# Kernel optimization log

Hardware: AMD Instinct MI355X
Metric: run time of the kernel (lower is better)

Reference implementation:

```python
import jax, jax.numpy as jnp
import numpy as np

V, C, L, D = 16384, 16, 6, 64  # n_vars, max_clauses, max_variables, embedding_dim


def _normalize(x):
    # utils.normalize: L2-normalize along the feature axis
    return x / jnp.linalg.norm(x, axis=-1, keepdims=True)


def _rescombine(x, W1, b1, W2, b2):
    # ResidualCombine: normalize(sigmoid(layer1(x)) + layer2(x))
    h = jax.nn.sigmoid(x @ W1 + b1) + x @ W2 + b2
    return _normalize(h)


def setup_inputs() -> dict:
    key = jax.random.key(0)
    ks = jax.random.split(key, 14)
    s = 0.05
    variables = jax.random.normal(ks[0], (V, D), jnp.float32)
    # literal variable indices; slot 0 of every clause is the owning variable i
    lits = jax.random.randint(ks[1], (V, C, L), 0, V)
    lits = lits.at[:, :, 0].set(jnp.arange(V)[:, None])
    neg_mask = jax.random.bernoulli(ks[2], 0.5, (V, C, L))
    # literal validity: at least 2 literals per clause, slot 0 always valid
    nvar = jax.random.randint(ks[3], (V, C), 2, L + 1)
    var_valid = jnp.arange(L)[None, None, :] < nvar[:, :, None]
    # clause validity: at least 1 clause per variable
    nclause = jax.random.randint(ks[4], (V,), 1, C + 1)
    clause_valid = jnp.arange(C)[None, :] < nclause[:, None]
    # params
    Wn = jax.random.normal(ks[5], (D, D), jnp.float32) * s
    bn = jnp.zeros((D,), jnp.float32)
    f = jax.random.normal(ks[6], (D,), jnp.float32)
    false_emb = f / jnp.linalg.norm(f)  # Embedding(1, D, max_norm=1.0)
    W1v = jax.random.normal(ks[7], (L * D, D), jnp.float32) * s
    b1v = jnp.zeros((D,), jnp.float32)
    W2v = jax.random.normal(ks[8], (L * D, D), jnp.float32) * s
    b2v = jnp.zeros((D,), jnp.float32)
    W1c = jax.random.normal(ks[9], (C * D, D), jnp.float32) * s
    b1c = jnp.zeros((D,), jnp.float32)
    W2c = jax.random.normal(ks[10], (C * D, D), jnp.float32) * s
    b2c = jnp.zeros((D,), jnp.float32)
    return dict(variables=variables, lits=lits, neg_mask=neg_mask, var_valid=var_valid,
                clause_valid=clause_valid, Wn=Wn, bn=bn, false_emb=false_emb,
                W1v=W1v, b1v=b1v, W2v=W2v, b2v=b2v, W1c=W1c, b1c=b1c, W2c=W2c, b2c=b2c)


def reference(variables, lits, neg_mask, var_valid, clause_valid,
              Wn, bn, false_emb, W1v, b1v, W2v, b2v, W1c, b1c, W2c, b2c):
    # gather literal embeddings: [V, C, L, D]
    g = variables[lits]
    # negation linear for negative literals
    v = jnp.where(neg_mask[..., None], g @ Wn + bn, g)
    # pad invalid literal slots with the 'false' embedding
    v = jnp.where(var_valid[..., None], v, false_emb)
    # variable_combiner over flattened [L*D]
    clause_emb = _rescombine(v.reshape(V, C, L * D), W1v, b1v, W2v, b2v)  # [V, C, D]
    # pad missing clauses with 'true' = negation(false)
    true_emb = false_emb @ Wn + bn
    clause_emb = jnp.where(clause_valid[..., None], clause_emb, true_emb)
    # clause_combiner over flattened [C*D]
    out = _rescombine(clause_emb.reshape(V, C * D), W1c, b1c, W2c, b2c)  # [V, D]
    # variables with no clauses pass through unchanged
    has_clauses = clause_valid.any(axis=-1)
    return jnp.where(has_clauses[:, None], out, variables)
```

## Files before the change

### kernel.cpp

```cpp
#include <hip/hip_runtime.h>
#include <hip/hip_bf16.h>

#define NV 16384
#define NC 16
#define NL 6
#define ND 64

typedef unsigned short u16;
typedef unsigned int u32;
typedef __attribute__((ext_vector_type(8))) short short8;
typedef __attribute__((ext_vector_type(4))) float f32x4;

#define PB_BN  0
#define PB_FE  64
#define PB_B1V 128
#define PB_B2V 192
#define PB_B1C 256
#define PB_B2C 320
#define U_BVS   896
#define U_BCS   50048
#define U_BN    181120
#define U_VARSB 185216
#define U_NEGB  1233856
#define U_CES   2282496
#define U_FIDX  19059712

__device__ __forceinline__ float ldbf(const u16* p, int i) {
  return __uint_as_float(((u32)p[i]) << 16);
}
__device__ __forceinline__ u16 f2b(float f) {
  u32 x = __float_as_uint(f);
  return (u16)((x + 0x7FFF + ((x >> 16) & 1)) >> 16);
}
__device__ __forceinline__ int ldmask(const void* p, int i, int bdt) {
  return bdt ? (int)((const signed char*)p)[i] : ((const int*)p)[i];
}
__device__ __forceinline__ float ldf(const void* p, int i, int fdt) {
  return fdt ? ldbf((const u16*)p, i) : ((const float*)p)[i];
}
__device__ __forceinline__ void gll16(const u16* g, u16* l) {
  __builtin_amdgcn_global_load_lds(
      (const __attribute__((address_space(1))) u32*)(g),
      (__attribute__((address_space(3))) u32*)(l), 16, 0, 0);
}

__global__ __launch_bounds__(256) void k_prep(
    const void* vars, const int* __restrict__ lits, const void* negm, const void* vval,
    const void* Wn, const void* bn, const void* femb,
    const void* W1v, const void* b1v, const void* W2v, const void* b2v,
    const void* W1c, const void* b1c, const void* W2c, const void* b2c,
    int* flags, float* pbuf, u16* wsB) {
  __shared__ int s_cnt[4], s_big[4];
  const int t = threadIdx.x;
  {
    const u32 w = ((const u32*)vars)[t];
    const u32 e = (w >> 7) & 0xFF;
    const unsigned long long bal = __ballot(e >= 0x6E && e <= 0x8E);
    const u32 bw = ((const u32*)vval)[t];
    const unsigned long long bb = __ballot(bw > 1u);
    if ((t & 63) == 0) { s_cnt[t >> 6] = __popcll(bal); s_big[t >> 6] = (bb != 0ull); }
  }
  __syncthreads();
  const int fdt = (s_cnt[0] + s_cnt[1] + s_cnt[2] + s_cnt[3]) >= 192;
  const int bdt = (s_big[0] | s_big[1] | s_big[2] | s_big[3]);
  const int bid = blockIdx.x;

  if (bid == 0) {
    if (t == 0) { flags[0] = fdt; flags[1] = bdt; }
    if (t < 64) {
      const void* src[6] = {bn, femb, b1v, b2v, b1c, b2c};
      const int off[6] = {PB_BN, PB_FE, PB_B1V, PB_B2V, PB_B1C, PB_B2C};
      for (int j = 0; j < 6; j++) pbuf[off[j] + t] = ldf(src[j], t, fdt);
      wsB[U_VARSB + NV * 64 + t] = fdt ? ((const u16*)femb)[t] : f2b(((const float*)femb)[t]);
    }
    for (int i = t; i < 4096; i += 256) {
      const int n = i >> 6, k = i & 63;
      wsB[U_BN + i] = f2b(ldf(Wn, k * 64 + n, fdt));
    }
  } else if (bid < 25) {
    const int c = (bid - 1) * 256 + t;
    const int ln = c & 63, nt = (c >> 6) & 7, ks = c >> 9;
    const int n = nt * 16 + (ln & 15);
    const void* src = (n < 64) ? W1v : W2v;
    const int kb = ks * 32 + (ln >> 4) * 8, n6 = n & 63;
    u16 o[8];
#pragma unroll
    for (int j = 0; j < 8; j++) o[j] = f2b(ldf(src, (kb + j) * 64 + n6, fdt));
    *(short8*)(wsB + U_BVS + c * 8) = *(short8*)o;
  } else if (bid < 89) {
    const int c = (bid - 25) * 256 + t;
    const int ln = c & 63, nt = (c >> 6) & 7, ks = c >> 9;
    const int n = nt * 16 + (ln & 15);
    const void* src = (n < 64) ? W1c : W2c;
    const int kb = ks * 32 + (ln >> 4) * 8, n6 = n & 63;
    u16 o[8];
#pragma unroll
    for (int j = 0; j < 8; j++) o[j] = f2b(ldf(src, (kb + j) * 64 + n6, fdt));
    *(short8*)(wsB + U_BCS + c * 8) = *(short8*)o;
  } else if (bid < 601) {
    const int c8 = (bid - 89) * 256 + t;
    u16 o[8];
    if (fdt) {
      *(short8*)o = ((const short8*)vars)[c8];
    } else {
      const float* f = (const float*)vars + c8 * 8;
#pragma unroll
      for (int j = 0; j < 8; j++) o[j] = f2b(f[j]);
    }
    *(short8*)(wsB + U_VARSB + c8 * 8) = *(short8*)o;
  } else {
    const int i0 = ((bid - 601) * 256 + t) * 4;
    u16 o[4];
#pragma unroll
    for (int j = 0; j < 4; j++) {
      const int i = i0 + j;
      const int valid = ldmask(vval, i, bdt);
      const int neg = ldmask(negm, i, bdt);
      const int idx = lits[i];
      o[j] = (u16)(valid ? (idx + (neg ? (NV + 1) : 0)) : NV);
    }
    *(ushort4*)(wsB + U_FIDX + i0) = *(ushort4*)o;
  }
}

__global__ __launch_bounds__(256) void k_negvar(const float* pbuf, u16* wsB) {
  const int tid = threadIdx.x, lane = tid & 63, wv = tid >> 6;
  const int col = lane & 15, quad = lane >> 4, q8 = quad * 8;
  const int rowbase = blockIdx.x * 64 + wv * 16;
  f32x4 acc[4];
#pragma unroll
  for (int nt = 0; nt < 4; nt++) acc[nt] = (f32x4){0.f, 0.f, 0.f, 0.f};
  const int arow = min(rowbase + col, NV);
#pragma unroll
  for (int ks = 0; ks < 2; ks++) {
    const short8 a = *(const short8*)(wsB + U_VARSB + arow * 64 + ks * 32 + q8);
#pragma unroll
    for (int nt = 0; nt < 4; nt++) {
      const short8 b = *(const short8*)(wsB + U_BN + (nt * 16 + col) * 64 + ks * 32 + q8);
      acc[nt] = __builtin_amdgcn_mfma_f32_16x16x32_bf16(a, b, acc[nt], 0, 0, 0);
    }
  }
#pragma unroll
  for (int reg = 0; reg < 4; reg++) {
    const int r = rowbase + quad * 4 + reg;
    if (r <= NV) {
#pragma unroll
      for (int nt = 0; nt < 4; nt++) {
        const int d = nt * 16 + col;
        wsB[U_NEGB + r * 64 + d] = f2b(acc[nt][reg] + pbuf[PB_BN + d]);
      }
    }
  }
}

__global__ __launch_bounds__(256, 2) void k_clause(
    const void* __restrict__ cval, const float* __restrict__ pbuf,
    const int* __restrict__ flags, u16* __restrict__ wsB) {
  __shared__ __align__(16) u16 Bs[2][12288];

  const int tid = threadIdx.x, lane = tid & 63, wv = tid >> 6;
  const int col = lane & 15, quad = lane >> 4, q8 = quad * 8;
  const int bdt = flags[1];
  const int vbase = (blockIdx.x * 4 + wv) * 4;

  u32 r2_[4][3];
#pragma unroll
  for (int v4 = 0; v4 < 4; v4++)
#pragma unroll
    for (int i = 0; i < 3; i++)
      r2_[4 > v4 ? v4 : 0][i] = *(const u32*)(wsB + U_FIDX + (vbase + v4) * 96 + col * 6 + i * 2);

  const int cv = ldmask(cval, vbase * 16 + lane, bdt);
  const unsigned long long bal = __ballot(cv != 0);

  f32x4 acc[4][8];
#pragma unroll
  for (int v4 = 0; v4 < 4; v4++)
#pragma unroll
    for (int nt = 0; nt < 8; nt++) acc[v4][nt] = (f32x4){0.f, 0.f, 0.f, 0.f};

#pragma unroll
  for (int j = 0; j < 6; j++) {
    const int cl = wv * 6 + j;
    gll16(wsB + U_BVS + cl * 512 + lane * 8, &Bs[0][cl * 512]);
  }
  short8 a_cur[4], a_nxt[4];
#pragma unroll
  for (int v4 = 0; v4 < 4; v4++) {
    const int idx = (int)(r2_[v4][0] & 0xFFFFu);
    a_cur[v4] = *(const short8*)(wsB + U_VARSB + idx * 64 + q8);
  }
  __syncthreads();

  for (int q = 0; q < 4; q++) {
    if (q < 3) {
#pragma unroll
      for (int j = 0; j < 6; j++) {
        const int cl = wv * 6 + j;
        gll16(wsB + U_BVS + (q + 1) * 12288 + cl * 512 + lane * 8, &Bs[(q + 1) & 1][cl * 512]);
      }
    }
#pragma unroll
    for (int ksl = 0; ksl < 3; ksl++) {
      const int gk = q * 3 + ksl;
      if (gk < 11) {
        const int gn = gk + 1;
        const int goff = (gn & 1) * 32 + q8;
        const int pi = gn >> 2, ph = (gn >> 1) & 1;
#pragma unroll
        for (int v4 = 0; v4 < 4; v4++) {
          const int idx = (int)((r2_[v4][pi] >> (ph * 16)) & 0xFFFFu);
          a_nxt[v4] = *(const short8*)(wsB + U_VARSB + idx * 64 + goff);
        }
      }
#pragma unroll
      for (int nt = 0; nt < 8; nt++) {
        const short8 b = *(const short8*)(&Bs[q & 1][(ksl * 8 + nt) * 512 + lane * 8]);
#pragma unroll
        for (int v4 = 0; v4 < 4; v4++)
          acc[v4][nt] = __builtin_amdgcn_mfma_f32_16x16x32_bf16(a_cur[v4], b, acc[v4][nt], 0, 0, 0);
      }
#pragma unroll
      for (int v4 = 0; v4 < 4; v4++) a_cur[v4] = a_nxt[v4];
    }
    if (q < 3) __syncthreads();
  }

  float b1l[4], b2l[4], truel[4];
#pragma unroll
  for (int nt = 0; nt < 4; nt++) {
    const int d = nt * 16 + col;
    b1l[nt] = pbuf[PB_B1V + d];
    b2l[nt] = pbuf[PB_B2V + d];
    truel[nt] = ldbf(wsB, U_NEGB + NV * 64 + d);
  }
#pragma unroll
  for (int v4 = 0; v4 < 4; v4++) {
    const u32 vmask = (u32)((bal >> (v4 * 16)) & 0xFFFFull);
    const int vloc = wv * 4 + v4;
#pragma unroll
    for (int reg = 0; reg < 4; reg++) {
      const int c = quad * 4 + reg;
      float hh[4], ss = 0.f;
#pragma unroll
      for (int nt = 0; nt < 4; nt++) {
        hh[nt] = 1.0f / (1.0f + __expf(-(acc[v4][nt][reg] + b1l[nt]))) + acc[v4][nt + 4][reg] + b2l[nt];
        ss += hh[nt] * hh[nt];
      }
      ss += __shfl_xor(ss, 1, 64); ss += __shfl_xor(ss, 2, 64);
      ss += __shfl_xor(ss, 4, 64); ss += __shfl_xor(ss, 8, 64);
      const float sc = 1.0f / sqrtf(ss);
      const int valid = (vmask >> c) & 1;
#pragma unroll
      for (int nt = 0; nt < 4; nt++) {
        const float o = valid ? hh[nt] * sc : truel[nt];
        const int l2 = (nt * 2 + (col >> 3)) & 3;
        wsB[U_CES + ((blockIdx.x * 32 + c * 2 + (nt >> 1)) * 64 + l2 * 16 + vloc) * 8 + (col & 7)] = f2b(o);
      }
    }
  }
}

__global__ __launch_bounds__(512) void k_var(
    const void* __restrict__ vars, const void* __restrict__ cval,
    const float* __restrict__ pbuf, const int* __restrict__ flags,
    const u16* __restrict__ wsB, void* __restrict__ outv) {
  __shared__ __align__(16) u16 Xs[32768];
  __shared__ float ps[32][4];
  __shared__ int hcS[32];

  const int tid = threadIdx.x, lane = tid & 63, wv = tid >> 6;
  const int col = lane & 15, quad = lane >> 4;
  const int fdt = flags[0], bdt = flags[1];
  const int v0 = blockIdx.x * 32;
  const int mt = wv >> 2, nq = wv & 3;

#pragma unroll
  for (int j = 0; j < 8; j++) {
    const int c = wv * 8 + j;
    gll16(wsB + U_CES + blockIdx.x * 32768 + c * 512 + lane * 8, &Xs[c * 512]);
  }
  {
    const int cv = ldmask(cval, v0 * NC + tid, bdt);
    const unsigned long long bal = __ballot(cv != 0);
    const int u = lane >> 4;
    if ((lane & 15) == 0) hcS[wv * 4 + u] = (int)((bal >> (u * 16)) & 0xFFFFull) != 0;
  }
  __syncthreads();

  f32x4 acc1 = (f32x4){0.f, 0.f, 0.f, 0.f}, acc2 = (f32x4){0.f, 0.f, 0.f, 0.f};
#pragma unroll 8
  for (int ks = 0; ks < 32; ks++) {
    const short8 a = *(const short8*)(&Xs[(mt * 32 + ks) * 512 + lane * 8]);
    const short8 b1 = *(const short8*)(wsB + U_BCS + (ks * 8 + nq) * 512 + lane * 8);
    const short8 b2 = *(const short8*)(wsB + U_BCS + (ks * 8 + nq + 4) * 512 + lane * 8);
    acc1 = __builtin_amdgcn_mfma_f32_16x16x32_bf16(a, b1, acc1, 0, 0, 0);
    acc2 = __builtin_amdgcn_mfma_f32_16x16x32_bf16(a, b2, acc2, 0, 0, 0);
  }

  const int d = nq * 16 + col;
  const float b1c_d = pbuf[PB_B1C + d], b2c_d = pbuf[PB_B2C + d];
  float h[4];
#pragma unroll
  for (int reg = 0; reg < 4; reg++) {
    h[reg] = 1.0f / (1.0f + __expf(-(acc1[reg] + b1c_d))) + acc2[reg] + b2c_d;
    float ssp = h[reg] * h[reg];
    ssp += __shfl_xor(ssp, 1, 64); ssp += __shfl_xor(ssp, 2, 64);
    ssp += __shfl_xor(ssp, 4, 64); ssp += __shfl_xor(ssp, 8, 64);
    if (col == 0) ps[mt * 16 + quad * 4 + reg][nq] = ssp;
  }
  __syncthreads();
#pragma unroll
  for (int reg = 0; reg < 4; reg++) {
    const int r = mt * 16 + quad * 4 + reg;
    const int v = v0 + r;
    const float tot = ps[r][0] + ps[r][1] + ps[r][2] + ps[r][3];
    float o = h[reg] * (1.0f / sqrtf(tot));
    const int oi = v * 64 + d;
    if (hcS[r]) {
      if (fdt) ((u16*)outv)[oi] = f2b(o);
      else ((float*)outv)[oi] = o;
    } else {
      if (fdt) ((u16*)outv)[oi] = ((const u16*)vars)[oi];
      else ((float*)outv)[oi] = ((const float*)vars)[oi];
    }
  }
}

extern "C" void kernel_launch(void* const* d_in, const int* in_sizes, int n_in,
                              void* d_out, int out_size, void* d_ws, size_t ws_size,
                              hipStream_t stream) {
  const void* vars = d_in[0];
  const int* lits = (const int*)d_in[1];
  const void* negm = d_in[2];
  const void* vval = d_in[3];
  const void* cvalid = d_in[4];
  const void* Wn = d_in[5];
  const void* bn = d_in[6];
  const void* femb = d_in[7];
  const void* W1v = d_in[8];
  const void* b1v = d_in[9];
  const void* W2v = d_in[10];
  const void* b2v = d_in[11];
  const void* W1c = d_in[12];
  const void* b1c = d_in[13];
  const void* W2c = d_in[14];
  const void* b2c = d_in[15];

  int* flags = (int*)d_ws;
  float* pbuf = (float*)((char*)d_ws + 256);
  u16* wsB = (u16*)d_ws;

  k_prep<<<2137, 256, 0, stream>>>(vars, lits, negm, vval, Wn, bn, femb,
                                   W1v, b1v, W2v, b2v, W1c, b1c, W2c, b2c,
                                   flags, pbuf, wsB);
  k_negvar<<<(NV + 1 + 63) / 64, 256, 0, stream>>>(pbuf, wsB);
  k_clause<<<NV / 16, 256, 0, stream>>>(cvalid, pbuf, flags, wsB);
  k_var<<<NV / 32, 512, 0, stream>>>(vars, cvalid, pbuf, flags, wsB, d_out);
}
```

Measured before the change: 168.7 us.

## Fuse clause and variable combiner kernels, keeping clause embeddings in LDS

Merges k_clause and k_var into one kernel. Each 16-variable block writes its normalized clause embeddings into the shared-memory buffer it already uses for staging weights, then runs the clause-combiner GEMM directly from LDS. This drops the workspace round trip for the clause-embedding tensor (about 33 MB of bf16 written and read back) and one kernel launch. In exchange, the second GEMM now works on 16 rows per block instead of 32, so the clause-combiner weights are read from global memory twice as often per variable.

```diff
diff --git a/kernel.cpp b/kernel.cpp
--- a/kernel.cpp
+++ b/kernel.cpp
@@ -22,8 +22,7 @@
 #define U_BN    181120
 #define U_VARSB 185216
 #define U_NEGB  1233856
-#define U_CES   2282496
-#define U_FIDX  19059712
+#define U_FIDX  2282496
 
 __device__ __forceinline__ float ldbf(const u16* p, int i) {
   return __uint_as_float(((u32)p[i]) << 16);
@@ -153,25 +152,30 @@
   }
 }
 
-__global__ __launch_bounds__(256, 2) void k_clause(
-    const void* __restrict__ cval, const float* __restrict__ pbuf,
-    const int* __restrict__ flags, u16* __restrict__ wsB) {
-  __shared__ __align__(16) u16 Bs[2][12288];
+__global__ __launch_bounds__(256, 2) void k_main(
+    const void* __restrict__ vars, const void* __restrict__ cval,
+    const float* __restrict__ pbuf, const int* __restrict__ flags,
+    const u16* __restrict__ wsB, void* __restrict__ outv) {
+  __shared__ __align__(16) u16 smem[24576];
+  __shared__ float ps[16][4];
+  __shared__ int hcS[16];
 
   const int tid = threadIdx.x, lane = tid & 63, wv = tid >> 6;
   const int col = lane & 15, quad = lane >> 4, q8 = quad * 8;
-  const int bdt = flags[1];
+  const int fdt = flags[0], bdt = flags[1];
   const int vbase = (blockIdx.x * 4 + wv) * 4;
+  const int v0 = blockIdx.x * 16;
 
   u32 r2_[4][3];
 #pragma unroll
   for (int v4 = 0; v4 < 4; v4++)
 #pragma unroll
     for (int i = 0; i < 3; i++)
-      r2_[4 > v4 ? v4 : 0][i] = *(const u32*)(wsB + U_FIDX + (vbase + v4) * 96 + col * 6 + i * 2);
+      r2_[v4][i] = *(const u32*)(wsB + U_FIDX + (vbase + v4) * 96 + col * 6 + i * 2);
 
   const int cv = ldmask(cval, vbase * 16 + lane, bdt);
   const unsigned long long bal = __ballot(cv != 0);
+  if (lane < 4) hcS[wv * 4 + lane] = ((bal >> (lane * 16)) & 0xFFFFull) != 0;
 
   f32x4 acc[4][8];
 #pragma unroll
@@ -182,7 +186,7 @@
 #pragma unroll
   for (int j = 0; j < 6; j++) {
     const int cl = wv * 6 + j;
-    gll16(wsB + U_BVS + cl * 512 + lane * 8, &Bs[0][cl * 512]);
+    gll16(wsB + U_BVS + cl * 512 + lane * 8, &smem[cl * 512]);
   }
   short8 a_cur[4], a_nxt[4];
 #pragma unroll
@@ -197,7 +201,8 @@
 #pragma unroll
       for (int j = 0; j < 6; j++) {
         const int cl = wv * 6 + j;
-        gll16(wsB + U_BVS + (q + 1) * 12288 + cl * 512 + lane * 8, &Bs[(q + 1) & 1][cl * 512]);
+        gll16(wsB + U_BVS + (q + 1) * 12288 + cl * 512 + lane * 8,
+              &smem[((q + 1) & 1) * 12288 + cl * 512]);
       }
     }
 #pragma unroll
@@ -215,7 +220,7 @@
       }
 #pragma unroll
       for (int nt = 0; nt < 8; nt++) {
-        const short8 b = *(const short8*)(&Bs[q & 1][(ksl * 8 + nt) * 512 + lane * 8]);
+        const short8 b = *(const short8*)(&smem[(q & 1) * 12288 + (ksl * 8 + nt) * 512 + lane * 8]);
 #pragma unroll
         for (int v4 = 0; v4 < 4; v4++)
           acc[v4][nt] = __builtin_amdgcn_mfma_f32_16x16x32_bf16(a_cur[v4], b, acc[v4][nt], 0, 0, 0);
@@ -225,80 +230,56 @@
     }
     if (q < 3) __syncthreads();
   }
-
-  float b1l[4], b2l[4], truel[4];
-#pragma unroll
-  for (int nt = 0; nt < 4; nt++) {
-    const int d = nt * 16 + col;
-    b1l[nt] = pbuf[PB_B1V + d];
-    b2l[nt] = pbuf[PB_B2V + d];
-    truel[nt] = ldbf(wsB, U_NEGB + NV * 64 + d);
-  }
-#pragma unroll
-  for (int v4 = 0; v4 < 4; v4++) {
-    const u32 vmask = (u32)((bal >> (v4 * 16)) & 0xFFFFull);
-    const int vloc = wv * 4 + v4;
-#pragma unroll
-    for (int reg = 0; reg < 4; reg++) {
-      const int c = quad * 4 + reg;
-      float hh[4], ss = 0.f;
-#pragma unroll
-      for (int nt = 0; nt < 4; nt++) {
-        hh[nt] = 1.0f / (1.0f + __expf(-(acc[v4][nt][reg] + b1l[nt]))) + acc[v4][nt + 4][reg] + b2l[nt];
-        ss += hh[nt] * hh[nt];
-      }
-      ss += __shfl_xor(ss, 1, 64); ss += __shfl_xor(ss, 2, 64);
-      ss += __shfl_xor(ss, 4, 64); ss += __shfl_xor(ss, 8, 64);
-      const float sc = 1.0f / sqrtf(ss);
-      const int valid = (vmask >> c) & 1;
-#pragma unroll
-      for (int nt = 0; nt < 4; nt++) {
-        const float o = valid ? hh[nt] * sc : truel[nt];
-        const int l2 = (nt * 2 + (col >> 3)) & 3;
-        wsB[U_CES + ((blockIdx.x * 32 + c * 2 + (nt >> 1)) * 64 + l2 * 16 + vloc) * 8 + (col & 7)] = f2b(o);
-      }
-    }
-  }
-}
-
-__global__ __launch_bounds__(512) void k_var(
-    const void* __restrict__ vars, const void* __restrict__ cval,
-    const float* __restrict__ pbuf, const int* __restrict__ flags,
-    const u16* __restrict__ wsB, void* __restrict__ outv) {
-  __shared__ __align__(16) u16 Xs[32768];
-  __shared__ float ps[32][4];
-  __shared__ int hcS[32];
-
-  const int tid = threadIdx.x, lane = tid & 63, wv = tid >> 6;
-  const int col = lane & 15, quad = lane >> 4;
-  const int fdt = flags[0], bdt = flags[1];
-  const int v0 = blockIdx.x * 32;
-  const int mt = wv >> 2, nq = wv & 3;
-
-#pragma unroll
-  for (int j = 0; j < 8; j++) {
-    const int c = wv * 8 + j;
-    gll16(wsB + U_CES + blockIdx.x * 32768 + c * 512 + lane * 8, &Xs[c * 512]);
-  }
+  __syncthreads();
+
   {
-    const int cv = ldmask(cval, v0 * NC + tid, bdt);
-    const unsigned long long bal = __ballot(cv != 0);
-    const int u = lane >> 4;
-    if ((lane & 15) == 0) hcS[wv * 4 + u] = (int)((bal >> (u * 16)) & 0xFFFFull) != 0;
+    float b1l[4], b2l[4], truel[4];
+#pragma unroll
+    for (int nt = 0; nt < 4; nt++) {
+      const int d = nt * 16 + col;
+      b1l[nt] = pbuf[PB_B1V + d];
+      b2l[nt] = pbuf[PB_B2V + d];
+      truel[nt] = ldbf(wsB, U_NEGB + NV * 64 + d);
+    }
+#pragma unroll
+    for (int v4 = 0; v4 < 4; v4++) {
+      const u32 vmask = (u32)((bal >> (v4 * 16)) & 0xFFFFull);
+      const int vloc = wv * 4 + v4;
+#pragma unroll
+      for (int reg = 0; reg < 4; reg++) {
+        const int c = quad * 4 + reg;
+        float hh[4], ss = 0.f;
+#pragma unroll
+        for (int nt = 0; nt < 4; nt++) {
+          hh[nt] = 1.0f / (1.0f + __expf(-(acc[v4][nt][reg] + b1l[nt]))) + acc[v4][nt + 4][reg] + b2l[nt];
+          ss += hh[nt] * hh[nt];
+        }
+        ss += __shfl_xor(ss, 1, 64); ss += __shfl_xor(ss, 2, 64);
+        ss += __shfl_xor(ss, 4, 64); ss += __shfl_xor(ss, 8, 64);
+        const float sc = 1.0f / sqrtf(ss);
+        const int valid = (vmask >> c) & 1;
+#pragma unroll
+        for (int nt = 0; nt < 4; nt++) {
+          const float o = valid ? hh[nt] * sc : truel[nt];
+          const int l2 = (nt * 2 + (col >> 3)) & 3;
+          smem[(c * 2 + (nt >> 1)) * 512 + (l2 * 16 + vloc) * 8 + (col & 7)] = f2b(o);
+        }
+      }
+    }
   }
   __syncthreads();
 
   f32x4 acc1 = (f32x4){0.f, 0.f, 0.f, 0.f}, acc2 = (f32x4){0.f, 0.f, 0.f, 0.f};
 #pragma unroll 8
   for (int ks = 0; ks < 32; ks++) {
-    const short8 a = *(const short8*)(&Xs[(mt * 32 + ks) * 512 + lane * 8]);
-    const short8 b1 = *(const short8*)(wsB + U_BCS + (ks * 8 + nq) * 512 + lane * 8);
-    const short8 b2 = *(const short8*)(wsB + U_BCS + (ks * 8 + nq + 4) * 512 + lane * 8);
+    const short8 a = *(const short8*)(&smem[ks * 512 + lane * 8]);
+    const short8 b1 = *(const short8*)(wsB + U_BCS + (ks * 8 + wv) * 512 + lane * 8);
+    const short8 b2 = *(const short8*)(wsB + U_BCS + (ks * 8 + wv + 4) * 512 + lane * 8);
     acc1 = __builtin_amdgcn_mfma_f32_16x16x32_bf16(a, b1, acc1, 0, 0, 0);
     acc2 = __builtin_amdgcn_mfma_f32_16x16x32_bf16(a, b2, acc2, 0, 0, 0);
   }
 
-  const int d = nq * 16 + col;
+  const int d = wv * 16 + col;
   const float b1c_d = pbuf[PB_B1C + d], b2c_d = pbuf[PB_B2C + d];
   float h[4];
 #pragma unroll
@@ -307,16 +288,15 @@
     float ssp = h[reg] * h[reg];
     ssp += __shfl_xor(ssp, 1, 64); ssp += __shfl_xor(ssp, 2, 64);
     ssp += __shfl_xor(ssp, 4, 64); ssp += __shfl_xor(ssp, 8, 64);
-    if (col == 0) ps[mt * 16 + quad * 4 + reg][nq] = ssp;
+    if (col == 0) ps[quad * 4 + reg][wv] = ssp;
   }
   __syncthreads();
 #pragma unroll
   for (int reg = 0; reg < 4; reg++) {
-    const int r = mt * 16 + quad * 4 + reg;
-    const int v = v0 + r;
+    const int r = quad * 4 + reg;
     const float tot = ps[r][0] + ps[r][1] + ps[r][2] + ps[r][3];
     float o = h[reg] * (1.0f / sqrtf(tot));
-    const int oi = v * 64 + d;
+    const int oi = (v0 + r) * 64 + d;
     if (hcS[r]) {
       if (fdt) ((u16*)outv)[oi] = f2b(o);
       else ((float*)outv)[oi] = o;
@@ -355,6 +335,5 @@
                                    W1v, b1v, W2v, b2v, W1c, b1c, W2c, b2c,
                                    flags, pbuf, wsB);
   k_negvar<<<(NV + 1 + 63) / 64, 256, 0, stream>>>(pbuf, wsB);
-  k_clause<<<NV / 16, 256, 0, stream>>>(cvalid, pbuf, flags, wsB);
-  k_var<<<NV / 32, 512, 0, stream>>>(vars, cvalid, pbuf, flags, wsB, d_out);
-}
+  k_main<<<NV / 16, 256, 0, stream>>>(vars, cvalid, pbuf, flags, wsB, d_out);
+}
```

After: 158.3 us. 6.2% less time.
